# Kernel optimization log

Hardware: AMD Instinct MI355X
Metric: run time of the kernel (lower is better)

Reference implementation:

```python
import jax, jax.numpy as jnp
import numpy as np

N_ENT = 15000
N_REL = 237
HID = 128
N_STEP = 3
EPS = 1e-10
E_BASE = 200000
BATCH, NEG = 8, 16


def _lstm(x, w_ih, w_hh, b_ih, b_hh):
    # x: [T, B, H]; single-layer PyTorch-style LSTM (gate order i, f, g, o)
    B = x.shape[1]
    H = w_hh.shape[1]
    bias = b_ih + b_hh

    def step(carry, xt):
        h, c = carry
        gates = xt @ w_ih.T + h @ w_hh.T + bias  # [B, 4H]
        i, f, g, o = jnp.split(gates, 4, axis=-1)
        c = jax.nn.sigmoid(f) * c + jax.nn.sigmoid(i) * jnp.tanh(g)
        h = jax.nn.sigmoid(o) * jnp.tanh(c)
        return (h, c), h

    init = (jnp.zeros((B, H), x.dtype), jnp.zeros((B, H), x.dtype))
    _, hs = jax.lax.scan(step, init, x)
    return hs  # [T, B, H]


def setup_inputs() -> dict:
    key = jax.random.key(0)
    ks = jax.random.split(key, 16)
    h_index = jax.random.randint(ks[0], (BATCH, NEG), 0, N_ENT)
    t_index = jax.random.randint(ks[1], (BATCH, NEG), 0, N_ENT)
    r_index = jax.random.randint(ks[2], (BATCH, NEG), 0, N_REL)
    src = jax.random.randint(ks[3], (E_BASE,), 0, N_ENT)
    dst = jax.random.randint(ks[4], (E_BASE,), 0, N_ENT)
    rel = jax.random.randint(ks[5], (E_BASE,), 0, N_REL)
    edge_weight = jnp.ones((2 * E_BASE,), jnp.float32)
    s = 0.05
    query_emb = jax.random.normal(ks[6], (2 * N_REL + 1, HID), jnp.float32) * s
    w_ih = jax.random.normal(ks[7], (4 * HID, HID), jnp.float32) * s
    w_hh = jax.random.normal(ks[8], (4 * HID, HID), jnp.float32) * s
    b_ih = jax.random.normal(ks[9], (4 * HID,), jnp.float32) * s
    b_hh = jax.random.normal(ks[10], (4 * HID,), jnp.float32) * s
    weight_w = jax.random.normal(ks[11], (2 * N_REL, HID), jnp.float32) * s
    weight_b = jax.random.normal(ks[12], (2 * N_REL,), jnp.float32) * s
    lin_w = jax.random.normal(ks[13], (), jnp.float32)
    lin_b = jax.random.normal(ks[14], (), jnp.float32)
    return {"query_emb": query_emb, "w_ih": w_ih, "w_hh": w_hh, "b_ih": b_ih,
            "b_hh": b_hh, "weight_w": weight_w, "weight_b": weight_b,
            "lin_w": lin_w, "lin_b": lin_b, "edge_weight": edge_weight,
            "h_index": h_index, "t_index": t_index, "r_index": r_index,
            "src": src, "dst": dst, "rel": rel}


def reference(query_emb, w_ih, w_hh, b_ih, b_hh, weight_w, weight_b,
              lin_w, lin_b, edge_weight, h_index, t_index, r_index,
              src, dst, rel):
    R2 = 2 * N_REL
    # graph.undirected(add_inverse=True): add reversed edges with inverse relations
    node_in = jnp.concatenate([src, dst])
    node_out = jnp.concatenate([dst, src])
    relation = jnp.concatenate([rel, rel + N_REL])

    # negative_sample_to_tail
    is_t_neg = jnp.all(h_index == h_index[:, :1], axis=-1, keepdims=True)
    h_i = jnp.where(is_t_neg, h_index, t_index)
    t_i = jnp.where(is_t_neg, t_index, h_index)
    r_i = jnp.where(is_t_neg, r_index, r_index + N_REL)

    hr = (h_i * R2 + r_i).ravel()
    uniq, inv = jnp.unique(hr, return_inverse=True, size=hr.shape[0], fill_value=0)
    inv = inv.ravel().reshape(h_i.shape)
    h_set = uniq // R2
    r_set = uniq % R2
    B = uniq.shape[0]

    # query sequence: [r]*(T-1) + [end=R2]
    q_idx = jnp.concatenate([jnp.tile(r_set[None], (N_STEP - 1, 1)),
                             jnp.full((1, B), R2, r_set.dtype)], axis=0)
    query = query_emb[q_idx]                      # [T, B, H]
    hidden = _lstm(query, w_ih, w_hh, b_ih, b_hh)  # [T, B, H]

    memory = jax.nn.one_hot(h_set, N_ENT, dtype=query.dtype)[None]  # [1, B, N]
    out = None
    for i in range(N_STEP):
        k = hidden[i]                                   # [B, H]
        attn = jax.nn.softmax(jnp.einsum('bd,tbd->bt', k, hidden[:i + 1]), axis=-1)
        inp = jnp.einsum('bt,tbn->nb', attn, memory)    # [N, B]
        w = jax.nn.softmax(k @ weight_w.T + weight_b, axis=-1).T  # [R2, B]
        # gather -> relation-weight multiply -> scatter_add
        msg = inp[node_in] * w[relation] * edge_weight[:, None]   # [2E, B]
        out = jnp.zeros((N_ENT, B), inp.dtype).at[node_out].add(msg)
        out = out / jnp.maximum(out.sum(axis=0, keepdims=True), EPS)
        memory = jnp.concatenate([memory, out.T[None]], axis=0)

    score = out[t_i, inv]          # [batch, neg]
    return score * lin_w + lin_b
```

## Files before the change

### kernel.cpp

```cpp
#include <hip/hip_runtime.h>
#include <math.h>

#define N_ENT  15000
#define N_RELC 237
#define R2C    474
#define EBASE  200000
#define E2     400000
#define EPSV   1e-10f
#define CAP    72
#define NSLICE 64
#define CSTR   16

typedef unsigned int uint32;
typedef unsigned short ushort16;

__device__ __forceinline__ ushort16 f2bf(float x) {
    uint32 u = __float_as_uint(x);
    u = (u + 0x7FFFu + ((u >> 16) & 1u)) >> 16;
    return (ushort16)u;
}
__device__ __forceinline__ float bflo(uint32 u) { return __uint_as_float(u << 16); }
__device__ __forceinline__ float bfhi(uint32 u) { return __uint_as_float(u & 0xFFFF0000u); }
__device__ __forceinline__ uint32 pk2(float lo, float hi) {
    return (uint32)f2bf(lo) | ((uint32)f2bf(hi) << 16);
}

__global__ void init_kernel(float* __restrict__ out0, int* __restrict__ cursor,
                            float* __restrict__ Swide,
                            const float* __restrict__ w_ih, const float* __restrict__ w_hh,
                            const float* __restrict__ weight_w,
                            float* __restrict__ wit, float* __restrict__ wht,
                            float* __restrict__ wwt,
                            const int* __restrict__ h_index, const int* __restrict__ t_index,
                            const int* __restrict__ r_index,
                            int* __restrict__ h_set, int* __restrict__ r_set,
                            int* __restrict__ invp, int* __restrict__ t_flat,
                            int* __restrict__ headidx) {
    if (blockIdx.x == gridDim.x - 1) {
        __shared__ int sv[128], eq[128], f_[128], uniq[128], hsh[128];
        __shared__ int isneg[8];
        __shared__ int UcntS;
        int j = threadIdx.x;
        for (int idx = j; idx < N_ENT; idx += 256) headidx[idx] = -1;
        __syncthreads();
        int hrv = 0, first = 0, rank = 0;
        if (j < 128) {
            int b = j >> 4;
            eq[j] = (h_index[j] == h_index[b * 16]) ? 1 : 0;
        }
        __syncthreads();
        if (j < 128 && (j & 15) == 0) {
            int b = j >> 4, a = 1;
            for (int q = 0; q < 16; q++) a &= eq[b * 16 + q];
            isneg[b] = a;
        }
        __syncthreads();
        if (j < 128) {
            int b = j >> 4;
            int h = h_index[j], t = t_index[j], r = r_index[j];
            int hi, ti, ri;
            if (isneg[b]) { hi = h; ti = t; ri = r; }
            else          { hi = t; ti = h; ri = r + N_RELC; }
            t_flat[j] = ti;
            hrv = hi * R2C + ri;
            sv[j] = hrv;
            uniq[j] = 0;
        }
        __syncthreads();
        if (j < 128) {
            first = 1;
            for (int q = 0; q < j; q++) if (sv[q] == hrv) { first = 0; break; }
            f_[j] = first;
        }
        __syncthreads();
        if (j < 128) {
            for (int q = 0; q < 128; q++) rank += (f_[q] && sv[q] < hrv) ? 1 : 0;
        }
        if (j == 0) {
            int c = 0;
            for (int q = 0; q < 128; q++) c += f_[q];
            UcntS = c;
        }
        __syncthreads();
        if (j < 128) {
            if (first) uniq[rank] = hrv;
            invp[j] = rank;
        }
        __syncthreads();
        if (j < 128) {
            int uv = uniq[j];
            h_set[j] = uv / R2C;
            r_set[j] = uv % R2C;
            hsh[j] = uv / R2C;
        }
        __syncthreads();
        if (j < 128) {
            int U = UcntS;
            int hs = hsh[j];
            if (j < U && (j == 0 || hsh[j - 1] != hs)) {
                int e = j + 1;
                while (e < U && hsh[e] == hs) e++;
                headidx[hs] = (j << 8) | e;
            }
        }
        return;
    }
    int idx = blockIdx.x * 256 + threadIdx.x;
    float4 z4 = make_float4(0.f, 0.f, 0.f, 0.f);
    if (idx < 480000) { ((float4*)out0)[idx] = z4; return; }
    idx -= 480000;
    if (idx < 60000) { ((int4*)cursor)[idx] = make_int4(0, 0, 0, 0); return; }
    idx -= 60000;
    if (idx < 6144) { ((float4*)Swide)[idx] = z4; return; }
    idx -= 6144;
    if (idx < 65536) {
        int d = idx >> 9, g = idx & 511;
        wit[idx] = w_ih[g * 128 + d];
        wht[idx] = w_hh[g * 128 + d];
        return;
    }
    idx -= 65536;
    if (idx < 65536) {
        int d = idx >> 9, r = idx & 511;
        if (r < R2C) wwt[idx] = weight_w[r * 128 + d];
    }
}

__global__ void lstm_kernel(const float* __restrict__ query_emb,
                            const int* __restrict__ r_set,
                            const float* __restrict__ wit, const float* __restrict__ wht,
                            const float* __restrict__ b_ih, const float* __restrict__ b_hh,
                            float* __restrict__ hidden) {
    int b = blockIdx.x, g = threadIdx.x;
    __shared__ float x[128], h[128], gl[512];
    float bias = b_ih[g] + b_hh[g];
    if (g < 128) x[g] = query_emb[r_set[b] * 128 + g];
    __syncthreads();
    float p0 = 0.f, p1 = 0.f, p2 = 0.f, p3 = 0.f;
    #pragma unroll 8
    for (int d = 0; d < 128; d += 4) {
        p0 += x[d + 0] * wit[(d + 0) * 512 + g];
        p1 += x[d + 1] * wit[(d + 1) * 512 + g];
        p2 += x[d + 2] * wit[(d + 2) * 512 + g];
        p3 += x[d + 3] * wit[(d + 3) * 512 + g];
    }
    float xpA = bias + ((p0 + p1) + (p2 + p3));
    __syncthreads();
    if (g < 128) x[g] = query_emb[R2C * 128 + g];
    __syncthreads();
    p0 = p1 = p2 = p3 = 0.f;
    #pragma unroll 8
    for (int d = 0; d < 128; d += 4) {
        p0 += x[d + 0] * wit[(d + 0) * 512 + g];
        p1 += x[d + 1] * wit[(d + 1) * 512 + g];
        p2 += x[d + 2] * wit[(d + 2) * 512 + g];
        p3 += x[d + 3] * wit[(d + 3) * 512 + g];
    }
    float xpB = bias + ((p0 + p1) + (p2 + p3));
    if (g < 128) h[g] = 0.f;
    float c = 0.f;
    __syncthreads();
    for (int step = 0; step < 3; step++) {
        float a0 = 0.f, a1 = 0.f, a2 = 0.f, a3 = 0.f;
        #pragma unroll 8
        for (int d = 0; d < 128; d += 4) {
            a0 += h[d + 0] * wht[(d + 0) * 512 + g];
            a1 += h[d + 1] * wht[(d + 1) * 512 + g];
            a2 += h[d + 2] * wht[(d + 2) * 512 + g];
            a3 += h[d + 3] * wht[(d + 3) * 512 + g];
        }
        gl[g] = ((step < 2) ? xpA : xpB) + ((a0 + a1) + (a2 + a3));
        __syncthreads();
        if (g < 128) {
            float ig = gl[g], fg = gl[128 + g], gg = gl[256 + g], og = gl[384 + g];
            float si = 1.f / (1.f + expf(-ig));
            float sf = 1.f / (1.f + expf(-fg));
            float so = 1.f / (1.f + expf(-og));
            c = sf * c + si * tanhf(gg);
            float hh = so * tanhf(c);
            hidden[(step * 128 + b) * 128 + g] = hh;
            h[g] = hh;
        }
        __syncthreads();
    }
}

__global__ void fill_kernel(const int* __restrict__ src, const int* __restrict__ dst,
                            const int* __restrict__ rel, const float* __restrict__ ew,
                            int* __restrict__ cursor, int2* __restrict__ edata2) {
    int e = blockIdx.x * 256 + threadIdx.x;
    if (e >= E2) return;
    int ni, no, r;
    if (e < EBASE) { ni = src[e]; no = dst[e]; r = rel[e]; }
    else { int e2 = e - EBASE; ni = dst[e2]; no = src[e2]; r = rel[e2] + N_RELC; }
    float w = ew[e];
    int pos = atomicAdd(&cursor[no * CSTR], 1);
    if (pos < CAP)
        edata2[no * CAP + pos] = make_int2((ni << 9) | r, __float_as_int(w));
}

__global__ void coef_kernel(const float* __restrict__ hidden, int step,
                            const float* __restrict__ Swide,
                            const float* __restrict__ wwt,
                            const float* __restrict__ weight_b,
                            ushort16* __restrict__ wTb, float* __restrict__ attnS) {
    int b = blockIdx.x, tid = threadIdx.x;
    __shared__ float k[128];
    __shared__ float red[256];
    __shared__ float sc[3];
    __shared__ float Ssum[2];
    __shared__ float logit[R2C];
    if (tid < 128) k[tid] = hidden[(step * 128 + b) * 128 + tid];
    __syncthreads();
    for (int t = 0; t <= step; t++) {
        float v = 0.f;
        if (tid < 128) v = k[tid] * hidden[(t * 128 + b) * 128 + tid];
        red[tid] = v;
        __syncthreads();
        for (int s2 = 128; s2 > 0; s2 >>= 1) {
            if (tid < s2) red[tid] += red[tid + s2];
            __syncthreads();
        }
        if (tid == 0) sc[t] = red[0];
        __syncthreads();
    }
    for (int t = 0; t < step; t++) {
        red[tid] = (tid < NSLICE) ? Swide[t * (NSLICE * 128) + tid * 128 + b] : 0.f;
        __syncthreads();
        for (int s2 = 128; s2 > 0; s2 >>= 1) {
            if (tid < s2) red[tid] += red[tid + s2];
            __syncthreads();
        }
        if (tid == 0) Ssum[t] = red[0];
        __syncthreads();
    }
    if (tid == 0) {
        float m = sc[0];
        for (int t2 = 1; t2 <= step; t2++) m = fmaxf(m, sc[t2]);
        float ssum = 0.f;
        float ex[3];
        for (int t2 = 0; t2 <= step; t2++) { ex[t2] = expf(sc[t2] - m); ssum += ex[t2]; }
        for (int t2 = 0; t2 <= step; t2++) {
            float a = ex[t2] / ssum;
            if (t2 > 0) a /= fmaxf(Ssum[t2 - 1], EPSV);
            attnS[b * 4 + t2] = a;
        }
    }
    for (int r = tid; r < R2C; r += 256) {
        float acc = weight_b[r];
        #pragma unroll 8
        for (int d = 0; d < 128; d++) acc += k[d] * wwt[d * 512 + r];
        logit[r] = acc;
    }
    __syncthreads();
    float m = -1e30f;
    for (int r = tid; r < R2C; r += 256) m = fmaxf(m, logit[r]);
    red[tid] = m; __syncthreads();
    for (int s2 = 128; s2 > 0; s2 >>= 1) {
        if (tid < s2) red[tid] = fmaxf(red[tid], red[tid + s2]);
        __syncthreads();
    }
    m = red[0]; __syncthreads();
    float s = 0.f;
    for (int r = tid; r < R2C; r += 256) s += expf(logit[r] - m);
    red[tid] = s; __syncthreads();
    for (int s2 = 128; s2 > 0; s2 >>= 1) {
        if (tid < s2) red[tid] += red[tid + s2];
        __syncthreads();
    }
    float invs = 1.f / red[0];
    for (int r = tid; r < R2C; r += 256)
        wTb[r * 128 + b] = f2bf(expf(logit[r] - m) * invs);
}

__global__ void step0_kernel(const int* __restrict__ src, const int* __restrict__ dst,
                             const int* __restrict__ rel, const float* __restrict__ ew,
                             const int* __restrict__ headidx,
                             const ushort16* __restrict__ wTb,
                             float* __restrict__ out0, float* __restrict__ Sw0) {
    int e = blockIdx.x * 256 + threadIdx.x;
    if (e >= E2) return;
    int ni, no, r;
    if (e < EBASE) { ni = src[e]; no = dst[e]; r = rel[e]; }
    else { int e2 = e - EBASE; ni = dst[e2]; no = src[e2]; r = rel[e2] + N_RELC; }
    int hv = headidx[ni];
    if (hv < 0) return;
    float w = ew[e];
    int b0 = hv >> 8, b1 = hv & 255;
    int sl = (e & (NSLICE - 1)) * 128;
    for (int b = b0; b < b1; b++) {
        float v = __uint_as_float(((uint32)wTb[r * 128 + b]) << 16) * w;
        atomicAdd(&out0[no * 128 + b], v);
        atomicAdd(&Sw0[sl + b], v);
    }
}

__global__ void inp_kernel(const float* __restrict__ o1, const ushort16* __restrict__ o2b,
                           int step, const float* __restrict__ attnS,
                           const int* __restrict__ h_set, ushort16* __restrict__ inpb) {
    int b = threadIdx.x;
    float a0 = attnS[b * 4 + 0];
    float a1 = attnS[b * 4 + 1];
    float a2 = (step >= 2) ? attnS[b * 4 + 2] : 0.f;
    int hs = h_set[b];
    for (int n = blockIdx.x; n < N_ENT; n += gridDim.x) {
        float v = (n == hs) ? a0 : 0.f;
        v += a1 * o1[n * 128 + b];
        if (step >= 2) v += a2 * __uint_as_float(((uint32)o2b[n * 128 + b]) << 16);
        inpb[n * 128 + b] = f2bf(v);
    }
}

template<int MODE>
__global__ void gather_kernel(const int2* __restrict__ edata2,
                              const int* __restrict__ cursor,
                              const ushort16* __restrict__ inpb,
                              const ushort16* __restrict__ wTb,
                              float* __restrict__ outf, ushort16* __restrict__ outb,
                              float* __restrict__ Sw) {
    __shared__ float sred[4][128];
    int wid = threadIdx.x >> 6;
    int lane = threadIdx.x & 63;
    int n = blockIdx.x * 4 + wid;
    int deg = cursor[n * CSTR];
    if (deg > CAP) deg = CAP;
    const int2* ed = edata2 + n * CAP;
    int c2 = lane * 2;
    float ax = 0.f, ay = 0.f;
    int e = 0;
    for (; e + 4 <= deg; e += 4) {
        int2 d0 = ed[e + 0], d1 = ed[e + 1], d2 = ed[e + 2], d3 = ed[e + 3];
        uint32 i0 = *(const uint32*)(inpb + ((d0.x >> 9) << 7) + c2);
        uint32 w0 = *(const uint32*)(wTb  + ((d0.x & 511) << 7) + c2);
        uint32 i1 = *(const uint32*)(inpb + ((d1.x >> 9) << 7) + c2);
        uint32 w1 = *(const uint32*)(wTb  + ((d1.x & 511) << 7) + c2);
        uint32 i2 = *(const uint32*)(inpb + ((d2.x >> 9) << 7) + c2);
        uint32 w2 = *(const uint32*)(wTb  + ((d2.x & 511) << 7) + c2);
        uint32 i3 = *(const uint32*)(inpb + ((d3.x >> 9) << 7) + c2);
        uint32 w3 = *(const uint32*)(wTb  + ((d3.x & 511) << 7) + c2);
        float f0 = __int_as_float(d0.y), f1 = __int_as_float(d1.y);
        float f2 = __int_as_float(d2.y), f3 = __int_as_float(d3.y);
        ax += bflo(i0) * bflo(w0) * f0 + bflo(i1) * bflo(w1) * f1
            + bflo(i2) * bflo(w2) * f2 + bflo(i3) * bflo(w3) * f3;
        ay += bfhi(i0) * bfhi(w0) * f0 + bfhi(i1) * bfhi(w1) * f1
            + bfhi(i2) * bfhi(w2) * f2 + bfhi(i3) * bfhi(w3) * f3;
    }
    for (; e < deg; e++) {
        int2 edv = ed[e];
        float w = __int_as_float(edv.y);
        uint32 ia = *(const uint32*)(inpb + ((edv.x >> 9) << 7) + c2);
        uint32 wa = *(const uint32*)(wTb  + ((edv.x & 511) << 7) + c2);
        ax += bflo(ia) * bflo(wa) * w;
        ay += bfhi(ia) * bfhi(wa) * w;
    }
    if (MODE == 0) {
        *(uint32*)((ushort16*)outb + (n << 7) + c2) = pk2(ax, ay);
    } else {
        *(float2*)(outf + n * 128 + c2) = make_float2(ax, ay);
    }
    sred[wid][c2] = ax;
    sred[wid][c2 + 1] = ay;
    __syncthreads();
    if (threadIdx.x < 128) {
        float s = sred[0][threadIdx.x] + sred[1][threadIdx.x]
                + sred[2][threadIdx.x] + sred[3][threadIdx.x];
        atomicAdd(&Sw[(blockIdx.x & (NSLICE - 1)) * 128 + threadIdx.x], s);
    }
}

__global__ void score_kernel(const float* __restrict__ out2, const float* __restrict__ Swide,
                             const int* __restrict__ t_flat, const int* __restrict__ invp,
                             const float* __restrict__ lin_w, const float* __restrict__ lin_b,
                             float* __restrict__ d_out) {
    int j = threadIdx.x;
    int bb = invp[j];
    float s = 0.f;
    for (int sl = 0; sl < NSLICE; sl++)
        s += Swide[2 * (NSLICE * 128) + sl * 128 + bb];
    d_out[j] = out2[t_flat[j] * 128 + bb] / fmaxf(s, EPSV) * lin_w[0] + lin_b[0];
}

extern "C" void kernel_launch(void* const* d_in, const int* in_sizes, int n_in,
                              void* d_out, int out_size, void* d_ws, size_t ws_size,
                              hipStream_t stream) {
    const float* query_emb  = (const float*)d_in[0];
    const float* w_ih       = (const float*)d_in[1];
    const float* w_hh       = (const float*)d_in[2];
    const float* b_ih       = (const float*)d_in[3];
    const float* b_hh       = (const float*)d_in[4];
    const float* weight_w   = (const float*)d_in[5];
    const float* weight_b   = (const float*)d_in[6];
    const float* lin_w      = (const float*)d_in[7];
    const float* lin_b      = (const float*)d_in[8];
    const float* edge_weight= (const float*)d_in[9];
    const int*   h_index    = (const int*)d_in[10];
    const int*   t_index    = (const int*)d_in[11];
    const int*   r_index    = (const int*)d_in[12];
    const int*   src        = (const int*)d_in[13];
    const int*   dst        = (const int*)d_in[14];
    const int*   rel        = (const int*)d_in[15];
    float* out = (float*)d_out;

    char* ws = (char*)d_ws;
    size_t off_b = 0;
    auto alloc = [&](size_t bytes) -> void* {
        void* p = ws + off_b;
        off_b = (off_b + bytes + 255) & ~(size_t)255;
        return p;
    };
    float*    hidden  = (float*)alloc(3 * 128 * 128 * sizeof(float));
    float*    attnS   = (float*)alloc(128 * 4 * sizeof(float));
    ushort16* wTb     = (ushort16*)alloc(R2C * 128 * sizeof(ushort16));
    float*    Swide   = (float*)alloc(3 * NSLICE * 128 * sizeof(float));
    float*    wit     = (float*)alloc(512 * 128 * sizeof(float));
    float*    wht     = (float*)alloc(512 * 128 * sizeof(float));
    float*    wwt     = (float*)alloc(512 * 128 * sizeof(float));
    int*      h_set   = (int*)alloc(128 * sizeof(int));
    int*      r_set   = (int*)alloc(128 * sizeof(int));
    int*      invp    = (int*)alloc(128 * sizeof(int));
    int*      t_flat  = (int*)alloc(128 * sizeof(int));
    int*      cursor  = (int*)alloc((size_t)N_ENT * CSTR * sizeof(int));
    int*      headidx = (int*)alloc(N_ENT * sizeof(int));
    int2*     edata2  = (int2*)alloc((size_t)N_ENT * CAP * sizeof(int2));
    ushort16* inpb    = (ushort16*)alloc((size_t)N_ENT * 128 * sizeof(ushort16));
    float*    outs0   = (float*)alloc((size_t)N_ENT * 128 * sizeof(float));
    ushort16* out1b   = (ushort16*)alloc((size_t)N_ENT * 128 * sizeof(ushort16));

    init_kernel<<<2647, 256, 0, stream>>>(outs0, cursor, Swide,
                                          w_ih, w_hh, weight_w, wit, wht, wwt,
                                          h_index, t_index, r_index,
                                          h_set, r_set, invp, t_flat, headidx);
    lstm_kernel<<<128, 512, 0, stream>>>(query_emb, r_set, wit, wht, b_ih, b_hh, hidden);
    fill_kernel<<<(E2 + 255) / 256, 256, 0, stream>>>(src, dst, rel, edge_weight,
                                                      cursor, edata2);

    coef_kernel<<<128, 256, 0, stream>>>(hidden, 0, Swide, wwt, weight_b, wTb, attnS);
    step0_kernel<<<(E2 + 255) / 256, 256, 0, stream>>>(src, dst, rel, edge_weight,
                                                       headidx, wTb, outs0, Swide);

    coef_kernel<<<128, 256, 0, stream>>>(hidden, 1, Swide, wwt, weight_b, wTb, attnS);
    inp_kernel<<<2048, 128, 0, stream>>>(outs0, out1b, 1, attnS, h_set, inpb);
    gather_kernel<0><<<N_ENT / 4, 256, 0, stream>>>(edata2, cursor, inpb, wTb,
                                                    nullptr, out1b, Swide + NSLICE * 128);

    coef_kernel<<<128, 256, 0, stream>>>(hidden, 2, Swide, wwt, weight_b, wTb, attnS);
    inp_kernel<<<2048, 128, 0, stream>>>(outs0, out1b, 2, attnS, h_set, inpb);
    gather_kernel<1><<<N_ENT / 4, 256, 0, stream>>>(edata2, cursor, inpb, wTb,
                                                    outs0, nullptr, Swide + 2 * NSLICE * 128);

    score_kernel<<<1, 128, 0, stream>>>(outs0, Swide, t_flat, invp, lin_w, lin_b, out);
}
```

Baseline: 166.8 us.

## Fuse score into last gather via completion counter and prefetch edge data

Removes the separate single-block score kernel launch by having the final gather kernel's last-finishing block compute the scores, using an atomic done counter zeroed in init. Also software-pipelines the edge-record loads in the gather loop so the next four edges are fetched while the current four are processed. This saves one launch and its gap, at the cost of a threadfence plus an atomic per block and slightly higher register pressure.

```diff
diff --git a/kernel.cpp b/kernel.cpp
--- a/kernel.cpp
+++ b/kernel.cpp
@@ -26,7 +26,7 @@
 }
 
 __global__ void init_kernel(float* __restrict__ out0, int* __restrict__ cursor,
-                            float* __restrict__ Swide,
+                            float* __restrict__ Swide, int* __restrict__ misc,
                             const float* __restrict__ w_ih, const float* __restrict__ w_hh,
                             const float* __restrict__ weight_w,
                             float* __restrict__ wit, float* __restrict__ wht,
@@ -113,6 +113,8 @@
     idx -= 60000;
     if (idx < 6144) { ((float4*)Swide)[idx] = z4; return; }
     idx -= 6144;
+    if (idx < 2) { ((int4*)misc)[idx] = make_int4(0, 0, 0, 0); return; }
+    idx -= 2;
     if (idx < 65536) {
         int d = idx >> 9, g = idx & 511;
         wit[idx] = w_ih[g * 128 + d];
@@ -311,14 +313,36 @@
     }
 }
 
+#define QPROC(d0, d1, d2, d3)                                                  \
+    do {                                                                       \
+        uint32 i0 = *(const uint32*)(inpb + (((d0).x >> 9) << 7) + c2);        \
+        uint32 w0 = *(const uint32*)(wTb  + (((d0).x & 511) << 7) + c2);       \
+        uint32 i1 = *(const uint32*)(inpb + (((d1).x >> 9) << 7) + c2);        \
+        uint32 w1 = *(const uint32*)(wTb  + (((d1).x & 511) << 7) + c2);       \
+        uint32 i2 = *(const uint32*)(inpb + (((d2).x >> 9) << 7) + c2);        \
+        uint32 w2 = *(const uint32*)(wTb  + (((d2).x & 511) << 7) + c2);       \
+        uint32 i3 = *(const uint32*)(inpb + (((d3).x >> 9) << 7) + c2);        \
+        uint32 w3 = *(const uint32*)(wTb  + (((d3).x & 511) << 7) + c2);       \
+        float f0 = __int_as_float((d0).y), f1 = __int_as_float((d1).y);        \
+        float f2 = __int_as_float((d2).y), f3 = __int_as_float((d3).y);        \
+        ax += bflo(i0) * bflo(w0) * f0 + bflo(i1) * bflo(w1) * f1              \
+            + bflo(i2) * bflo(w2) * f2 + bflo(i3) * bflo(w3) * f3;             \
+        ay += bfhi(i0) * bfhi(w0) * f0 + bfhi(i1) * bfhi(w1) * f1              \
+            + bfhi(i2) * bfhi(w2) * f2 + bfhi(i3) * bfhi(w3) * f3;             \
+    } while (0)
+
 template<int MODE>
 __global__ void gather_kernel(const int2* __restrict__ edata2,
                               const int* __restrict__ cursor,
                               const ushort16* __restrict__ inpb,
                               const ushort16* __restrict__ wTb,
                               float* __restrict__ outf, ushort16* __restrict__ outb,
-                              float* __restrict__ Sw) {
+                              float* __restrict__ Sw, int* __restrict__ done,
+                              const int* __restrict__ t_flat, const int* __restrict__ invp,
+                              const float* __restrict__ lin_w, const float* __restrict__ lin_b,
+                              float* __restrict__ d_out) {
     __shared__ float sred[4][128];
+    __shared__ int lastf;
     int wid = threadIdx.x >> 6;
     int lane = threadIdx.x & 63;
     int n = blockIdx.x * 4 + wid;
@@ -328,22 +352,15 @@
     int c2 = lane * 2;
     float ax = 0.f, ay = 0.f;
     int e = 0;
-    for (; e + 4 <= deg; e += 4) {
-        int2 d0 = ed[e + 0], d1 = ed[e + 1], d2 = ed[e + 2], d3 = ed[e + 3];
-        uint32 i0 = *(const uint32*)(inpb + ((d0.x >> 9) << 7) + c2);
-        uint32 w0 = *(const uint32*)(wTb  + ((d0.x & 511) << 7) + c2);
-        uint32 i1 = *(const uint32*)(inpb + ((d1.x >> 9) << 7) + c2);
-        uint32 w1 = *(const uint32*)(wTb  + ((d1.x & 511) << 7) + c2);
-        uint32 i2 = *(const uint32*)(inpb + ((d2.x >> 9) << 7) + c2);
-        uint32 w2 = *(const uint32*)(wTb  + ((d2.x & 511) << 7) + c2);
-        uint32 i3 = *(const uint32*)(inpb + ((d3.x >> 9) << 7) + c2);
-        uint32 w3 = *(const uint32*)(wTb  + ((d3.x & 511) << 7) + c2);
-        float f0 = __int_as_float(d0.y), f1 = __int_as_float(d1.y);
-        float f2 = __int_as_float(d2.y), f3 = __int_as_float(d3.y);
-        ax += bflo(i0) * bflo(w0) * f0 + bflo(i1) * bflo(w1) * f1
-            + bflo(i2) * bflo(w2) * f2 + bflo(i3) * bflo(w3) * f3;
-        ay += bfhi(i0) * bfhi(w0) * f0 + bfhi(i1) * bfhi(w1) * f1
-            + bfhi(i2) * bfhi(w2) * f2 + bfhi(i3) * bfhi(w3) * f3;
+    if (deg >= 4) {
+        int2 a0 = ed[0], a1 = ed[1], a2 = ed[2], a3 = ed[3];
+        for (; e + 8 <= deg; e += 4) {
+            int2 b0 = ed[e + 4], b1 = ed[e + 5], b2 = ed[e + 6], b3 = ed[e + 7];
+            QPROC(a0, a1, a2, a3);
+            a0 = b0; a1 = b1; a2 = b2; a3 = b3;
+        }
+        QPROC(a0, a1, a2, a3);
+        e += 4;
     }
     for (; e < deg; e++) {
         int2 edv = ed[e];
@@ -366,18 +383,22 @@
                 + sred[2][threadIdx.x] + sred[3][threadIdx.x];
         atomicAdd(&Sw[(blockIdx.x & (NSLICE - 1)) * 128 + threadIdx.x], s);
     }
-}
-
-__global__ void score_kernel(const float* __restrict__ out2, const float* __restrict__ Swide,
-                             const int* __restrict__ t_flat, const int* __restrict__ invp,
-                             const float* __restrict__ lin_w, const float* __restrict__ lin_b,
-                             float* __restrict__ d_out) {
-    int j = threadIdx.x;
-    int bb = invp[j];
-    float s = 0.f;
-    for (int sl = 0; sl < NSLICE; sl++)
-        s += Swide[2 * (NSLICE * 128) + sl * 128 + bb];
-    d_out[j] = out2[t_flat[j] * 128 + bb] / fmaxf(s, EPSV) * lin_w[0] + lin_b[0];
+    if (MODE == 1) {
+        __threadfence();
+        __syncthreads();
+        if (threadIdx.x == 0)
+            lastf = (atomicAdd(done, 1) == (int)gridDim.x - 1);
+        __syncthreads();
+        if (lastf) {
+            __threadfence();
+            if (threadIdx.x < 128) {
+                int j = threadIdx.x, bb = invp[j];
+                float s = 0.f;
+                for (int sl = 0; sl < NSLICE; sl++) s += Sw[sl * 128 + bb];
+                d_out[j] = outf[t_flat[j] * 128 + bb] / fmaxf(s, EPSV) * lin_w[0] + lin_b[0];
+            }
+        }
+    }
 }
 
 extern "C" void kernel_launch(void* const* d_in, const int* in_sizes, int n_in,
@@ -421,12 +442,14 @@
     int*      t_flat  = (int*)alloc(128 * sizeof(int));
     int*      cursor  = (int*)alloc((size_t)N_ENT * CSTR * sizeof(int));
     int*      headidx = (int*)alloc(N_ENT * sizeof(int));
+    int*      misc    = (int*)alloc(8 * sizeof(int));
     int2*     edata2  = (int2*)alloc((size_t)N_ENT * CAP * sizeof(int2));
     ushort16* inpb    = (ushort16*)alloc((size_t)N_ENT * 128 * sizeof(ushort16));
     float*    outs0   = (float*)alloc((size_t)N_ENT * 128 * sizeof(float));
     ushort16* out1b   = (ushort16*)alloc((size_t)N_ENT * 128 * sizeof(ushort16));
-
-    init_kernel<<<2647, 256, 0, stream>>>(outs0, cursor, Swide,
+    int* done = misc;
+
+    init_kernel<<<2647, 256, 0, stream>>>(outs0, cursor, Swide, misc,
                                           w_ih, w_hh, weight_w, wit, wht, wwt,
                                           h_index, t_index, r_index,
                                           h_set, r_set, invp, t_flat, headidx);
@@ -441,12 +464,12 @@
     coef_kernel<<<128, 256, 0, stream>>>(hidden, 1, Swide, wwt, weight_b, wTb, attnS);
     inp_kernel<<<2048, 128, 0, stream>>>(outs0, out1b, 1, attnS, h_set, inpb);
     gather_kernel<0><<<N_ENT / 4, 256, 0, stream>>>(edata2, cursor, inpb, wTb,
-                                                    nullptr, out1b, Swide + NSLICE * 128);
+                                                    nullptr, out1b, Swide + NSLICE * 128,
+                                                    done, t_flat, invp, lin_w, lin_b, out);
 
     coef_kernel<<<128, 256, 0, stream>>>(hidden, 2, Swide, wwt, weight_b, wTb, attnS);
     inp_kernel<<<2048, 128, 0, stream>>>(outs0, out1b, 2, attnS, h_set, inpb);
     gather_kernel<1><<<N_ENT / 4, 256, 0, stream>>>(edata2, cursor, inpb, wTb,
-                                                    outs0, nullptr, Swide + 2 * NSLICE * 128);
-
-    score_kernel<<<1, 128, 0, stream>>>(outs0, Swide, t_flat, invp, lin_w, lin_b, out);
-}
+                                                    outs0, nullptr, Swide + 2 * NSLICE * 128,
+                                                    done, t_flat, invp, lin_w, lin_b, out);
+}
```

After: 434.7 us. 2.61x slower.
